# Kernel optimization log

Measured on AMD Instinct MI355X. Metric: run time of the kernel, lower is better.

The kernel has to match this reference:

```python
import jax, jax.numpy as jnp
import numpy as np

KH, KW = 3, 3
STRIDE = (1, 1)
PAD = (1, 1)
DIL = (1, 1)


def setup_inputs() -> dict:
    key = jax.random.key(0)
    k1, k2, k3, k4 = jax.random.split(key, 4)
    B, Cin, H, W = 8, 256, 64, 64
    Cout = 256
    x = jax.random.normal(k1, (B, Cin, H, W), jnp.float32)
    offset = jax.random.normal(k2, (B, 2 * KH * KW, H, W), jnp.float32)
    fan_in = Cin * KH * KW
    bound = 1.0 / np.sqrt(fan_in).astype(np.float32)
    weight = jax.random.uniform(k3, (Cout, Cin, KH, KW), jnp.float32, -bound, bound)
    bias = jax.random.uniform(k4, (Cout,), jnp.float32, -bound, bound)
    return {"x": x, "offset": offset, "weight": weight, "bias": bias}


def _deform_conv2d(x, offset, weight, bias):
    B, Cin, H, W = x.shape
    Cout = weight.shape[0]
    Ho, Wo = offset.shape[2], offset.shape[3]
    # offset layout: [B, 2*KH*KW, Ho, Wo] -> (dy, dx) per kernel tap
    off = offset.reshape(B, KH, KW, 2, Ho, Wo)
    dy = off[:, :, :, 0]  # [B,KH,KW,Ho,Wo]
    dx = off[:, :, :, 1]
    grid_y = jnp.arange(Ho, dtype=x.dtype) * STRIDE[0] - PAD[0]  # [Ho]
    grid_x = jnp.arange(Wo, dtype=x.dtype) * STRIDE[1] - PAD[1]  # [Wo]
    ker_y = jnp.arange(KH, dtype=x.dtype) * DIL[0]  # [KH]
    ker_x = jnp.arange(KW, dtype=x.dtype) * DIL[1]  # [KW]
    # sampling positions [B,KH,KW,Ho,Wo]
    py = dy + grid_y[None, None, None, :, None] + ker_y[None, :, None, None, None]
    px = dx + grid_x[None, None, None, None, :] + ker_x[None, None, :, None, None]

    y0f = jnp.floor(py)
    x0f = jnp.floor(px)
    wy = py - y0f  # fractional weights
    wx = px - x0f
    y0 = y0f.astype(jnp.int32)
    x0 = x0f.astype(jnp.int32)

    x_flat = x.reshape(B, Cin, H * W)

    def corner(yi, xi, w):
        # bilinear corner with zero padding outside the image
        valid = (yi >= 0) & (yi < H) & (xi >= 0) & (xi < W)
        idx = jnp.clip(yi, 0, H - 1) * W + jnp.clip(xi, 0, W - 1)  # [B,KH,KW,Ho,Wo]
        vals = jax.vmap(lambda xf, ii: xf[:, ii])(x_flat, idx)  # [B,Cin,KH,KW,Ho,Wo]
        return vals * (w * valid)[:, None]

    acc = corner(y0, x0, (1 - wy) * (1 - wx))
    acc = acc + corner(y0, x0 + 1, (1 - wy) * wx)
    acc = acc + corner(y0 + 1, x0, wy * (1 - wx))
    acc = acc + corner(y0 + 1, x0 + 1, wy * wx)

    # convolution accumulation over (Cin, KH, KW)
    out = jnp.einsum('bckluv,ockl->bouv', acc, weight)
    return out + bias[None, :, None, None]


def reference(x, offset, weight, bias):
    return _deform_conv2d(x, offset, weight, bias)
```

## Files before the change

### kernel.cpp

```cpp
#include <hip/hip_runtime.h>
#include <hip/hip_bf16.h>
#include <stdint.h>

typedef __attribute__((ext_vector_type(8))) short s16x8;
typedef __attribute__((ext_vector_type(4))) float f32x4;

#define XT_OFF   0u
#define WT_OFF   16777216u
#define PW_OFF   17956864u
#define PI_OFF   22675456u
#define WS_NEED  25034752u

static __device__ __forceinline__ uint16_t f2bf(float f) {
    __hip_bfloat16 h = __float2bfloat16(f);
    uint16_t u;
    __builtin_memcpy(&u, &h, 2);
    return u;
}
static __device__ __forceinline__ float bflo(uint32_t w) { return __uint_as_float(w << 16); }
static __device__ __forceinline__ float bfhi(uint32_t w) { return __uint_as_float(w & 0xffff0000u); }

__global__ __launch_bounds__(256) void k_transpose_x(const float* __restrict__ x,
                                                     uint16_t* __restrict__ xt) {
    __shared__ float tile[64][65];
    const int blk = blockIdx.x;
    const int b   = blk >> 8;
    const int yxt = (blk >> 2) & 63;
    const int ct  = blk & 3;
    const int yx0 = yxt << 6, c0 = ct << 6;
    const int tx  = threadIdx.x;
    const int ty  = tx >> 6, lx = tx & 63;
    #pragma unroll
    for (int i = 0; i < 16; ++i) {
        const int c = (i << 2) + ty;
        tile[c][lx] = x[(size_t)((b * 256 + c0 + c) << 12) + yx0 + lx];
    }
    __syncthreads();
    const int cpr = lx & 31;
    #pragma unroll
    for (int i = 0; i < 8; ++i) {
        const int r = (ty << 1) + (lx >> 5) + (i << 3);
        const uint32_t lo = f2bf(tile[2 * cpr][r]);
        const uint32_t hi = f2bf(tile[2 * cpr + 1][r]);
        *(uint32_t*)&xt[(size_t)(b * 4096 + yx0 + r) * 256 + c0 + 2 * cpr] = lo | (hi << 16);
    }
}

__global__ __launch_bounds__(256) void k_prep_w(const float* __restrict__ wgt,
                                                uint16_t* __restrict__ wt) {
    const int o = blockIdx.x;
    const int c = threadIdx.x;
    #pragma unroll
    for (int t = 0; t < 9; ++t) {
        const float v = wgt[(size_t)o * 2304 + c * 9 + t];
        const int kb = t * 8 + (c >> 5);
        const int kk = c & 31;
        const uint32_t byte = (uint32_t)kb * 16384u + (uint32_t)o * 64u
            + (uint32_t)(((((kk >> 3) ^ ((o >> 1) & 3)) << 4)) | ((kk & 7) << 1));
        wt[byte >> 1] = f2bf(v);
    }
}

__global__ __launch_bounds__(256) void k_prep_params(const float* __restrict__ off,
                                                     float4* __restrict__ pw,
                                                     uint2* __restrict__ pi) {
    const int blk = blockIdx.x;
    const int b = blk / 144;
    const int r = blk - b * 144;
    const int t = r >> 4;
    const int p = ((r & 15) << 8) + threadIdx.x;
    const int u = p >> 6, v = p & 63;
    const int kh = t / 3, kw = t - 3 * kh;
    const float dy = off[(size_t)((b * 18 + 2 * t) << 12) + p];
    const float dx = off[(size_t)((b * 18 + 2 * t + 1) << 12) + p];
    const float py = dy + (float)(u - 1 + kh);
    const float px = dx + (float)(v - 1 + kw);
    const float y0f = floorf(py), x0f = floorf(px);
    const float wy = py - y0f, wx = px - x0f;
    const int y0 = (int)y0f, x0 = (int)x0f;
    const int y1 = y0 + 1, x1 = x0 + 1;
    const bool vy0 = (y0 >= 0) && (y0 < 64);
    const bool vy1 = (y1 >= 0) && (y1 < 64);
    const bool vx0 = (x0 >= 0) && (x0 < 64);
    const bool vx1 = (x1 >= 0) && (x1 < 64);
    const int cy0 = min(max(y0, 0), 63), cy1 = min(max(y1, 0), 63);
    const int cx0 = min(max(x0, 0), 63), cx1 = min(max(x1, 0), 63);
    float4 w4;
    w4.x = (1.f - wy) * (1.f - wx) * ((vy0 && vx0) ? 1.f : 0.f);
    w4.y = (1.f - wy) * wx         * ((vy0 && vx1) ? 1.f : 0.f);
    w4.z = wy * (1.f - wx)         * ((vy1 && vx0) ? 1.f : 0.f);
    w4.w = wy * wx                 * ((vy1 && vx1) ? 1.f : 0.f);
    uint2 id;
    id.x = (uint32_t)(cy0 * 64 + cx0) | ((uint32_t)(cy0 * 64 + cx1) << 16);
    id.y = (uint32_t)(cy1 * 64 + cx0) | ((uint32_t)(cy1 * 64 + cx1) << 16);
    const size_t o_ = (size_t)(b * 9 + t) * 4096 + p;
    pw[o_] = w4;
    pi[o_] = id;
}

#define W_DMA(KB, BUF) do {                                                       \
    const char* gw_ = (const char*)wt + (size_t)(KB) * 16384u;                    \
    char* lw_ = (char*)&w_lds[BUF][0];                                            \
    _Pragma("unroll")                                                             \
    for (int it_ = 0; it_ < 2; ++it_) {                                           \
        const int seg_ = wv * 2 + it_;                                            \
        __builtin_amdgcn_global_load_lds(                                         \
            (const __attribute__((address_space(1))) void*)(gw_ + seg_ * 1024 + lane * 16), \
            (__attribute__((address_space(3))) void*)(lw_ + seg_ * 1024), 16, 0, 0); \
    }                                                                             \
} while (0)

__global__ __launch_bounds__(512, 4) void k_main(const uint16_t* __restrict__ xt,
                                                 const uint16_t* __restrict__ wt,
                                                 const float4* __restrict__ pw,
                                                 const uint2* __restrict__ pi,
                                                 const float* __restrict__ bias,
                                                 float* __restrict__ out) {
    __shared__ uint16_t w_lds[3][8192];
    __shared__ uint16_t im2col[64 * 256];

    const int orig = blockIdx.x;
    const int bid  = (orig & 7) * 64 + (orig >> 3);
    const int b    = bid >> 6;
    const int pix0 = (bid & 63) << 6;

    const int tx   = threadIdx.x;
    const int lane = tx & 63;
    const int wv   = tx >> 6;
    const int wc   = wv & 3;
    const int wp   = wv >> 2;
    const int l15  = lane & 15;
    const int kp   = lane >> 4;

    const int ar    = wc * 64 + l15;
    const int a_off = ar * 64 + ((kp ^ ((ar >> 1) & 3)) << 4);

    const uint16_t* xb = xt + (size_t)b * 4096 * 256;

    f32x4 acc[4][2];
    #pragma unroll
    for (int m = 0; m < 4; ++m)
        #pragma unroll
        for (int j = 0; j < 2; ++j) acc[m][j] = (f32x4){0.f, 0.f, 0.f, 0.f};

    W_DMA(0, 0);
    W_DMA(1, 1);

    for (int t = 0; t < 9; ++t) {
        __syncthreads();
        #pragma unroll
        for (int i = 0; i < 8; ++i) {
            const int lp = wv * 8 + i;
            const int uidx = __builtin_amdgcn_readfirstlane((b * 9 + t) * 4096 + pix0 + lp);
            const uint2  id = pi[uidx];
            const float4 w4 = pw[uidx];
            const uint16_t* p00 = xb + (id.x & 0xffffu) * 256u;
            const uint16_t* p01 = xb + (id.x >> 16)     * 256u;
            const uint16_t* p10 = xb + (id.y & 0xffffu) * 256u;
            const uint16_t* p11 = xb + (id.y >> 16)     * 256u;
            const uint2 A  = *(const uint2*)(p00 + lane * 4);
            const uint2 Bv = *(const uint2*)(p01 + lane * 4);
            const uint2 Cv = *(const uint2*)(p10 + lane * 4);
            const uint2 Dv = *(const uint2*)(p11 + lane * 4);
            uint2 r;
            {
                const float lo = w4.x * bflo(A.x) + w4.y * bflo(Bv.x)
                               + w4.z * bflo(Cv.x) + w4.w * bflo(Dv.x);
                const float hi = w4.x * bfhi(A.x) + w4.y * bfhi(Bv.x)
                               + w4.z * bfhi(Cv.x) + w4.w * bfhi(Dv.x);
                r.x = (uint32_t)f2bf(lo) | ((uint32_t)f2bf(hi) << 16);
            }
            {
                const float lo = w4.x * bflo(A.y) + w4.y * bflo(Bv.y)
                               + w4.z * bflo(Cv.y) + w4.w * bflo(Dv.y);
                const float hi = w4.x * bfhi(A.y) + w4.y * bfhi(Bv.y)
                               + w4.z * bfhi(Cv.y) + w4.w * bfhi(Dv.y);
                r.y = (uint32_t)f2bf(lo) | ((uint32_t)f2bf(hi) << 16);
            }
            const int slot = (lane >> 1) ^ (lp & 7);
            *(uint2*)((char*)im2col + lp * 512 + slot * 16 + (lane & 1) * 8) = r;
        }
        __syncthreads();

        #pragma unroll
        for (int s = 0; s < 8; ++s) {
            const int kb = t * 8 + s;
            if (t == 8 && s == 7) asm volatile("s_waitcnt vmcnt(0) lgkmcnt(0)" ::: "memory");
            else                  asm volatile("s_waitcnt vmcnt(2) lgkmcnt(0)" ::: "memory");
            __builtin_amdgcn_s_barrier();
            __builtin_amdgcn_sched_barrier(0);
            if (kb + 2 < 72) {
                const int ib = (kb + 2) % 3;
                W_DMA(kb + 2, ib);
            }
            const int cb = kb % 3;
            const char* wb = (const char*)&w_lds[cb][0];
            s16x8 afr[4], bfr[2];
            #pragma unroll
            for (int m = 0; m < 4; ++m) afr[m] = *(const s16x8*)(wb + a_off + m * 1024);
            #pragma unroll
            for (int j = 0; j < 2; ++j) {
                const int pix  = wp * 32 + j * 16 + l15;
                const int boff = pix * 512 + (((s * 4 + kp) ^ (l15 & 7)) << 4);
                bfr[j] = *(const s16x8*)((const char*)im2col + boff);
            }
            __builtin_amdgcn_s_setprio(1);
            #pragma unroll
            for (int m = 0; m < 4; ++m)
                #pragma unroll
                for (int j = 0; j < 2; ++j)
                    acc[m][j] = __builtin_amdgcn_mfma_f32_16x16x32_bf16(afr[m], bfr[j], acc[m][j], 0, 0, 0);
            __builtin_amdgcn_s_setprio(0);
        }
    }

    #pragma unroll
    for (int m = 0; m < 4; ++m) {
        #pragma unroll
        for (int q = 0; q < 4; ++q) {
            const int o = wc * 64 + m * 16 + kp * 4 + q;
            const float bv = bias[o];
            float* orow = out + (((size_t)(b * 256 + o)) << 12) + pix0 + wp * 32;
            #pragma unroll
            for (int j = 0; j < 2; ++j)
                orow[j * 16 + l15] = acc[m][j][q] + bv;
        }
    }
}

#define KTOT 2304
#define KCF  32
#define WROW 260
#define AROW 72

__global__ __launch_bounds__(256) void deform_conv_fallback(
    const float* __restrict__ x, const float* __restrict__ off,
    const float* __restrict__ wgt, const float* __restrict__ bias,
    float* __restrict__ out) {
    __shared__ float  w_lds[KCF][WROW];
    __shared__ float  a_lds[KCF][AROW];
    __shared__ int4   pidx[9][64];
    __shared__ float4 pwgt[9][64];
    const int tx = threadIdx.x;
    const int blk = blockIdx.x;
    const int b = blk >> 6, u = blk & 63;
    for (int item = tx; item < 9 * 64; item += 256) {
        const int t = item >> 6, p = item & 63;
        const int k = t / 3, l = t - 3 * k;
        const float dy = off[((b * 18 + 2 * t) << 12) + u * 64 + p];
        const float dx = off[((b * 18 + 2 * t + 1) << 12) + u * 64 + p];
        const float py = dy + (float)(u - 1 + k);
        const float px = dx + (float)(p - 1 + l);
        const float y0f = floorf(py), x0f = floorf(px);
        const float wy = py - y0f, wx = px - x0f;
        const int y0 = (int)y0f, x0 = (int)x0f, y1 = y0 + 1, x1 = x0 + 1;
        const bool vy0 = (y0 >= 0) && (y0 < 64), vy1 = (y1 >= 0) && (y1 < 64);
        const bool vx0 = (x0 >= 0) && (x0 < 64), vx1 = (x1 >= 0) && (x1 < 64);
        const int cy0 = min(max(y0, 0), 63), cy1 = min(max(y1, 0), 63);
        const int cx0 = min(max(x0, 0), 63), cx1 = min(max(x1, 0), 63);
        int4 id; id.x = cy0 * 64 + cx0; id.y = cy0 * 64 + cx1;
        id.z = cy1 * 64 + cx0; id.w = cy1 * 64 + cx1;
        float4 w4;
        w4.x = (1.f - wy) * (1.f - wx) * ((vy0 && vx0) ? 1.f : 0.f);
        w4.y = (1.f - wy) * wx * ((vy0 && vx1) ? 1.f : 0.f);
        w4.z = wy * (1.f - wx) * ((vy1 && vx0) ? 1.f : 0.f);
        w4.w = wy * wx * ((vy1 && vx1) ? 1.f : 0.f);
        pidx[t][p] = id; pwgt[t][p] = w4;
    }
    const int og = tx & 31, pgr = tx >> 5;
    float acc[8][8];
    #pragma unroll
    for (int j = 0; j < 8; ++j)
        #pragma unroll
        for (int q = 0; q < 8; ++q) acc[j][q] = 0.f;
    __syncthreads();
    for (int kb = 0; kb < 72; ++kb) {
        const int k0 = kb * KCF;
        #pragma unroll
        for (int it = 0; it < 8; ++it) {
            const int item = it * 256 + tx;
            const int o = item >> 3, jj = item & 7;
            const float4 v = *(const float4*)&wgt[o * KTOT + k0 + jj * 4];
            w_lds[jj * 4 + 0][o] = v.x; w_lds[jj * 4 + 1][o] = v.y;
            w_lds[jj * 4 + 2][o] = v.z; w_lds[jj * 4 + 3][o] = v.w;
        }
        #pragma unroll
        for (int it = 0; it < 8; ++it) {
            const int item = it * 256 + tx;
            const int kk = item >> 6, p = item & 63;
            const int kg = k0 + kk;
            const int c = kg / 9, t = kg - 9 * c;
            const float* plane = x + ((b * 256 + c) << 12);
            const int4 id = pidx[t][p];
            const float4 w4 = pwgt[t][p];
            float v = w4.x * plane[id.x] + w4.y * plane[id.y]
                    + w4.z * plane[id.z] + w4.w * plane[id.w];
            a_lds[kk][p] = v;
        }
        __syncthreads();
        #pragma unroll 2
        for (int kk = 0; kk < KCF; ++kk) {
            const float4 w0 = *(const float4*)&w_lds[kk][og * 8];
            const float4 w1 = *(const float4*)&w_lds[kk][og * 8 + 4];
            const float4 a0 = *(const float4*)&a_lds[kk][pgr * 8];
            const float4 a1 = *(const float4*)&a_lds[kk][pgr * 8 + 4];
            const float wv[8] = {w0.x, w0.y, w0.z, w0.w, w1.x, w1.y, w1.z, w1.w};
            const float av[8] = {a0.x, a0.y, a0.z, a0.w, a1.x, a1.y, a1.z, a1.w};
            #pragma unroll
            for (int j = 0; j < 8; ++j)
                #pragma unroll
                for (int q = 0; q < 8; ++q) acc[j][q] += wv[j] * av[q];
        }
        __syncthreads();
    }
    const int vb = pgr * 8;
    #pragma unroll
    for (int j = 0; j < 8; ++j) {
        const int o = og * 8 + j;
        const float bv = bias[o];
        float* op = out + ((b * 256 + o) << 12) + u * 64 + vb;
        float4 r0, r1;
        r0.x = acc[j][0] + bv; r0.y = acc[j][1] + bv; r0.z = acc[j][2] + bv; r0.w = acc[j][3] + bv;
        r1.x = acc[j][4] + bv; r1.y = acc[j][5] + bv; r1.z = acc[j][6] + bv; r1.w = acc[j][7] + bv;
        *(float4*)op = r0; *(float4*)(op + 4) = r1;
    }
}

extern "C" void kernel_launch(void* const* d_in, const int* in_sizes, int n_in,
                              void* d_out, int out_size, void* d_ws, size_t ws_size,
                              hipStream_t stream) {
    const float* x    = (const float*)d_in[0];
    const float* off  = (const float*)d_in[1];
    const float* wgt  = (const float*)d_in[2];
    const float* bias = (const float*)d_in[3];
    float* out = (float*)d_out;

    if (ws_size < WS_NEED) {
        deform_conv_fallback<<<dim3(512), dim3(256), 0, stream>>>(x, off, wgt, bias, out);
        return;
    }
    uint16_t* xt  = (uint16_t*)((char*)d_ws + XT_OFF);
    uint16_t* wtp = (uint16_t*)((char*)d_ws + WT_OFF);
    float4*   pwp = (float4*)((char*)d_ws + PW_OFF);
    uint2*    pip = (uint2*)((char*)d_ws + PI_OFF);

    k_transpose_x <<<dim3(2048), dim3(256), 0, stream>>>(x, xt);
    k_prep_w      <<<dim3(256),  dim3(256), 0, stream>>>(wgt, wtp);
    k_prep_params <<<dim3(1152), dim3(256), 0, stream>>>(off, pwp, pip);
    k_main        <<<dim3(512),  dim3(512), 0, stream>>>(xt, wtp, pwp, pip, bias, out);
}
```

Baseline: 98.86 us.

## Software-pipeline bilinear gather for next tap behind current tap's MFMA steps

Reorganizes the main loop so the parameter loads and four-corner gathers for tap t+1 are issued in bursts interleaved with the eight MFMA k-steps of tap t. Blended results are held in registers and written to the single im2col buffer after a barrier at the end of each tap. The aim is to hide gather latency and remove the exposed two-barrier gather phase per tap. In exchange it adds many live registers under a 512x4 launch bound, which risks spills, and it relies on hand-tuned vmcnt values that must match the exact load counts.

```diff
diff --git a/kernel.cpp b/kernel.cpp
--- a/kernel.cpp
+++ b/kernel.cpp
@@ -110,6 +110,82 @@
     }                                                                             \
 } while (0)
 
+#define KSTEP(KB, N) do {                                                         \
+    asm volatile("s_waitcnt vmcnt(" #N ") lgkmcnt(0)" ::: "memory");              \
+    __builtin_amdgcn_s_barrier();                                                 \
+    __builtin_amdgcn_sched_barrier(0);                                            \
+    if ((KB) + 2 < 72) W_DMA((KB) + 2, ((KB) + 2) % 3);                           \
+    {                                                                             \
+        const int s_ = (KB) & 7;                                                  \
+        const char* wb_ = (const char*)&w_lds[(KB) % 3][0];                       \
+        s16x8 afr[4], bfr[2];                                                     \
+        _Pragma("unroll")                                                         \
+        for (int m = 0; m < 4; ++m) afr[m] = *(const s16x8*)(wb_ + a_off + m * 1024); \
+        _Pragma("unroll")                                                         \
+        for (int j = 0; j < 2; ++j) {                                             \
+            const int pix_  = wp * 32 + j * 16 + l15;                             \
+            const int boff_ = pix_ * 512 + (((s_ * 4 + kp) ^ (l15 & 7)) << 4);    \
+            bfr[j] = *(const s16x8*)((const char*)im2col + boff_);                \
+        }                                                                         \
+        __builtin_amdgcn_s_setprio(1);                                            \
+        _Pragma("unroll")                                                         \
+        for (int m = 0; m < 4; ++m)                                               \
+            _Pragma("unroll")                                                     \
+            for (int j = 0; j < 2; ++j)                                           \
+                acc[m][j] = __builtin_amdgcn_mfma_f32_16x16x32_bf16(afr[m], bfr[j], acc[m][j], 0, 0, 0); \
+        __builtin_amdgcn_s_setprio(0);                                            \
+    }                                                                             \
+} while (0)
+
+#define CBURST(P0) do {                                                           \
+    _Pragma("unroll")                                                             \
+    for (int i = 0; i < 4; ++i) {                                                 \
+        const uint2 id_ = pin[(P0) + i];                                          \
+        cA[i] = *(const uint2*)(xb + (id_.x & 0xffffu) * 256u + lane * 4);        \
+        cB[i] = *(const uint2*)(xb + (id_.x >> 16)     * 256u + lane * 4);        \
+        cC[i] = *(const uint2*)(xb + (id_.y & 0xffffu) * 256u + lane * 4);        \
+        cD[i] = *(const uint2*)(xb + (id_.y >> 16)     * 256u + lane * 4);        \
+    }                                                                             \
+} while (0)
+
+#define CBLEND(P0) do {                                                           \
+    _Pragma("unroll")                                                             \
+    for (int i = 0; i < 4; ++i) {                                                 \
+        const float4 w4_ = pwn[(P0) + i];                                         \
+        uint2 r_;                                                                 \
+        { const float lo = w4_.x * bflo(cA[i].x) + w4_.y * bflo(cB[i].x)          \
+                         + w4_.z * bflo(cC[i].x) + w4_.w * bflo(cD[i].x);         \
+          const float hi = w4_.x * bfhi(cA[i].x) + w4_.y * bfhi(cB[i].x)          \
+                         + w4_.z * bfhi(cC[i].x) + w4_.w * bfhi(cD[i].x);         \
+          r_.x = (uint32_t)f2bf(lo) | ((uint32_t)f2bf(hi) << 16); }               \
+        { const float lo = w4_.x * bflo(cA[i].y) + w4_.y * bflo(cB[i].y)          \
+                         + w4_.z * bflo(cC[i].y) + w4_.w * bflo(cD[i].y);         \
+          const float hi = w4_.x * bfhi(cA[i].y) + w4_.y * bfhi(cB[i].y)          \
+                         + w4_.z * bfhi(cC[i].y) + w4_.w * bfhi(cD[i].y);         \
+          r_.y = (uint32_t)f2bf(lo) | ((uint32_t)f2bf(hi) << 16); }               \
+        rr[(P0) + i] = r_;                                                        \
+    }                                                                             \
+} while (0)
+
+#define LOAD_PARAMS(TT) do {                                                      \
+    _Pragma("unroll")                                                             \
+    for (int i = 0; i < 8; ++i) {                                                 \
+        const int lp_ = wv * 8 + i;                                               \
+        const int ui_ = __builtin_amdgcn_readfirstlane((b * 9 + (TT)) * 4096 + pix0 + lp_); \
+        pin[i] = pi[ui_];                                                         \
+        pwn[i] = pw[ui_];                                                         \
+    }                                                                             \
+} while (0)
+
+#define DS_WRITE_RR() do {                                                        \
+    _Pragma("unroll")                                                             \
+    for (int i = 0; i < 8; ++i) {                                                 \
+        const int lp_ = wv * 8 + i;                                               \
+        const int slot_ = (lane >> 1) ^ (lp_ & 7);                                \
+        *(uint2*)((char*)im2col + lp_ * 512 + slot_ * 16 + (lane & 1) * 8) = rr[i]; \
+    }                                                                             \
+} while (0)
+
 __global__ __launch_bounds__(512, 4) void k_main(const uint16_t* __restrict__ xt,
                                                  const uint16_t* __restrict__ wt,
                                                  const float4* __restrict__ pw,
@@ -137,82 +213,53 @@
 
     const uint16_t* xb = xt + (size_t)b * 4096 * 256;
 
+    uint2  pin[8];
+    float4 pwn[8];
+    uint2  cA[4], cB[4], cC[4], cD[4];
+    uint2  rr[8];
+
     f32x4 acc[4][2];
     #pragma unroll
     for (int m = 0; m < 4; ++m)
         #pragma unroll
         for (int j = 0; j < 2; ++j) acc[m][j] = (f32x4){0.f, 0.f, 0.f, 0.f};
 
+    LOAD_PARAMS(0);
+    CBURST(0);
+    asm volatile("s_waitcnt vmcnt(0)" ::: "memory");
+    CBLEND(0);
+    CBURST(4);
     W_DMA(0, 0);
     W_DMA(1, 1);
-
-    for (int t = 0; t < 9; ++t) {
-        __syncthreads();
-        #pragma unroll
-        for (int i = 0; i < 8; ++i) {
-            const int lp = wv * 8 + i;
-            const int uidx = __builtin_amdgcn_readfirstlane((b * 9 + t) * 4096 + pix0 + lp);
-            const uint2  id = pi[uidx];
-            const float4 w4 = pw[uidx];
-            const uint16_t* p00 = xb + (id.x & 0xffffu) * 256u;
-            const uint16_t* p01 = xb + (id.x >> 16)     * 256u;
-            const uint16_t* p10 = xb + (id.y & 0xffffu) * 256u;
-            const uint16_t* p11 = xb + (id.y >> 16)     * 256u;
-            const uint2 A  = *(const uint2*)(p00 + lane * 4);
-            const uint2 Bv = *(const uint2*)(p01 + lane * 4);
-            const uint2 Cv = *(const uint2*)(p10 + lane * 4);
-            const uint2 Dv = *(const uint2*)(p11 + lane * 4);
-            uint2 r;
-            {
-                const float lo = w4.x * bflo(A.x) + w4.y * bflo(Bv.x)
-                               + w4.z * bflo(Cv.x) + w4.w * bflo(Dv.x);
-                const float hi = w4.x * bfhi(A.x) + w4.y * bfhi(Bv.x)
-                               + w4.z * bfhi(Cv.x) + w4.w * bfhi(Dv.x);
-                r.x = (uint32_t)f2bf(lo) | ((uint32_t)f2bf(hi) << 16);
-            }
-            {
-                const float lo = w4.x * bflo(A.y) + w4.y * bflo(Bv.y)
-                               + w4.z * bflo(Cv.y) + w4.w * bflo(Dv.y);
-                const float hi = w4.x * bfhi(A.y) + w4.y * bfhi(Bv.y)
-                               + w4.z * bfhi(Cv.y) + w4.w * bfhi(Dv.y);
-                r.y = (uint32_t)f2bf(lo) | ((uint32_t)f2bf(hi) << 16);
-            }
-            const int slot = (lane >> 1) ^ (lp & 7);
-            *(uint2*)((char*)im2col + lp * 512 + slot * 16 + (lane & 1) * 8) = r;
-        }
-        __syncthreads();
-
-        #pragma unroll
-        for (int s = 0; s < 8; ++s) {
-            const int kb = t * 8 + s;
-            if (t == 8 && s == 7) asm volatile("s_waitcnt vmcnt(0) lgkmcnt(0)" ::: "memory");
-            else                  asm volatile("s_waitcnt vmcnt(2) lgkmcnt(0)" ::: "memory");
-            __builtin_amdgcn_s_barrier();
-            __builtin_amdgcn_sched_barrier(0);
-            if (kb + 2 < 72) {
-                const int ib = (kb + 2) % 3;
-                W_DMA(kb + 2, ib);
-            }
-            const int cb = kb % 3;
-            const char* wb = (const char*)&w_lds[cb][0];
-            s16x8 afr[4], bfr[2];
-            #pragma unroll
-            for (int m = 0; m < 4; ++m) afr[m] = *(const s16x8*)(wb + a_off + m * 1024);
-            #pragma unroll
-            for (int j = 0; j < 2; ++j) {
-                const int pix  = wp * 32 + j * 16 + l15;
-                const int boff = pix * 512 + (((s * 4 + kp) ^ (l15 & 7)) << 4);
-                bfr[j] = *(const s16x8*)((const char*)im2col + boff);
-            }
-            __builtin_amdgcn_s_setprio(1);
-            #pragma unroll
-            for (int m = 0; m < 4; ++m)
-                #pragma unroll
-                for (int j = 0; j < 2; ++j)
-                    acc[m][j] = __builtin_amdgcn_mfma_f32_16x16x32_bf16(afr[m], bfr[j], acc[m][j], 0, 0, 0);
-            __builtin_amdgcn_s_setprio(0);
-        }
-    }
+    asm volatile("s_waitcnt vmcnt(4)" ::: "memory");
+    CBLEND(4);
+    DS_WRITE_RR();
+
+    #pragma unroll 1
+    for (int t = 0; t < 8; ++t) {
+        LOAD_PARAMS(t + 1);
+        CBURST(0);
+        KSTEP(t * 8 + 0, 18);
+        KSTEP(t * 8 + 1, 18);
+        KSTEP(t * 8 + 2, 2);
+        KSTEP(t * 8 + 3, 2);
+        asm volatile("s_waitcnt vmcnt(4)" ::: "memory");
+        CBLEND(0);
+        CBURST(4);
+        KSTEP(t * 8 + 4, 18);
+        KSTEP(t * 8 + 5, 18);
+        KSTEP(t * 8 + 6, 2);
+        KSTEP(t * 8 + 7, 2);
+        asm volatile("s_waitcnt vmcnt(4)" ::: "memory");
+        CBLEND(4);
+        asm volatile("s_waitcnt lgkmcnt(0)" ::: "memory");
+        __builtin_amdgcn_s_barrier();
+        __builtin_amdgcn_sched_barrier(0);
+        DS_WRITE_RR();
+    }
+
+    KSTEP(64, 2); KSTEP(65, 2); KSTEP(66, 2); KSTEP(67, 2);
+    KSTEP(68, 2); KSTEP(69, 2); KSTEP(70, 2); KSTEP(71, 0);
 
     #pragma unroll
     for (int m = 0; m < 4; ++m) {
```

Measured after the change: 115.8 us. +17.2%, slower.

## Software-pipeline deformable gather with MFMA, load weights directly into registers

Applied to the files above, without the earlier changes.

The main kernel is restructured so each block covers 128 pixels with a double-buffered im2col in LDS. The bilinear gather and blend for the next kernel tap is interleaved with the MFMA steps of the current tap, which removes the serial gather-then-compute phases. Weights are pre-packed into MFMA fragment order, so each wave loads its A fragments straight from global memory into registers instead of staging them through LDS with DMA. This larger tile raises per-thread register use and halves the grid to 256 blocks, trading occupancy for more reuse and overlap.

```diff
diff --git a/kernel.cpp b/kernel.cpp
--- a/kernel.cpp
+++ b/kernel.cpp
@@ -19,6 +19,9 @@
 }
 static __device__ __forceinline__ float bflo(uint32_t w) { return __uint_as_float(w << 16); }
 static __device__ __forceinline__ float bfhi(uint32_t w) { return __uint_as_float(w & 0xffff0000u); }
+static __device__ __forceinline__ float rdl(float v, int l) {
+    return __uint_as_float((uint32_t)__builtin_amdgcn_readlane((int)__float_as_uint(v), l));
+}
 
 __global__ __launch_bounds__(256) void k_transpose_x(const float* __restrict__ x,
                                                      uint16_t* __restrict__ xt) {
@@ -48,17 +51,21 @@
 
 __global__ __launch_bounds__(256) void k_prep_w(const float* __restrict__ wgt,
                                                 uint16_t* __restrict__ wt) {
-    const int o = blockIdx.x;
-    const int c = threadIdx.x;
-    #pragma unroll
-    for (int t = 0; t < 9; ++t) {
-        const float v = wgt[(size_t)o * 2304 + c * 9 + t];
-        const int kb = t * 8 + (c >> 5);
-        const int kk = c & 31;
-        const uint32_t byte = (uint32_t)kb * 16384u + (uint32_t)o * 64u
-            + (uint32_t)(((((kk >> 3) ^ ((o >> 1) & 3)) << 4)) | ((kk & 7) << 1));
-        wt[byte >> 1] = f2bf(v);
-    }
+    const int blk = blockIdx.x;
+    const int kb = blk >> 2, wc = blk & 3;
+    const int m = threadIdx.x >> 6, lane = threadIdx.x & 63;
+    const int o = wc * 64 + m * 16 + (lane & 15);
+    const int t = kb >> 3;
+    const int ch0 = (kb & 7) * 32 + (lane >> 4) * 8;
+    uint32_t pk[4];
+    #pragma unroll
+    for (int q = 0; q < 4; ++q) {
+        const float v0 = wgt[(size_t)o * 2304 + (size_t)(ch0 + 2 * q) * 9 + t];
+        const float v1 = wgt[(size_t)o * 2304 + (size_t)(ch0 + 2 * q + 1) * 9 + t];
+        pk[q] = (uint32_t)f2bf(v0) | ((uint32_t)f2bf(v1) << 16);
+    }
+    uint4 r; r.x = pk[0]; r.y = pk[1]; r.z = pk[2]; r.w = pk[3];
+    *(uint4*)((char*)wt + (size_t)kb * 16384 + wc * 4096 + m * 1024 + lane * 16) = r;
 }
 
 __global__ __launch_bounds__(256) void k_prep_params(const float* __restrict__ off,
@@ -98,120 +105,158 @@
     pi[o_] = id;
 }
 
-#define W_DMA(KB, BUF) do {                                                       \
-    const char* gw_ = (const char*)wt + (size_t)(KB) * 16384u;                    \
-    char* lw_ = (char*)&w_lds[BUF][0];                                            \
-    _Pragma("unroll")                                                             \
-    for (int it_ = 0; it_ < 2; ++it_) {                                           \
-        const int seg_ = wv * 2 + it_;                                            \
-        __builtin_amdgcn_global_load_lds(                                         \
-            (const __attribute__((address_space(1))) void*)(gw_ + seg_ * 1024 + lane * 16), \
-            (__attribute__((address_space(3))) void*)(lw_ + seg_ * 1024), 16, 0, 0); \
+
+#define BLENDPX(PAR, IDX, LP, PXL) do {                                           \
+    const float wqa = rdl(pwv.x, (PXL)), wqb = rdl(pwv.y, (PXL));                 \
+    const float wqc = rdl(pwv.z, (PXL)), wqd = rdl(pwv.w, (PXL));                 \
+    const uint2 A_ = cr[PAR][(IDX)*4+0], B_ = cr[PAR][(IDX)*4+1];                 \
+    const uint2 C_ = cr[PAR][(IDX)*4+2], D_ = cr[PAR][(IDX)*4+3];                 \
+    uint2 r_;                                                                     \
+    { const float lo = wqa * bflo(A_.x) + wqb * bflo(B_.x)                        \
+                     + wqc * bflo(C_.x) + wqd * bflo(D_.x);                       \
+      const float hi = wqa * bfhi(A_.x) + wqb * bfhi(B_.x)                        \
+                     + wqc * bfhi(C_.x) + wqd * bfhi(D_.x);                       \
+      r_.x = (uint32_t)f2bf(lo) | ((uint32_t)f2bf(hi) << 16); }                   \
+    { const float lo = wqa * bflo(A_.y) + wqb * bflo(B_.y)                        \
+                     + wqc * bflo(C_.y) + wqd * bflo(D_.y);                       \
+      const float hi = wqa * bfhi(A_.y) + wqb * bfhi(B_.y)                        \
+                     + wqc * bfhi(C_.y) + wqd * bfhi(D_.y);                       \
+      r_.y = (uint32_t)f2bf(lo) | ((uint32_t)f2bf(hi) << 16); }                   \
+    const int slot_ = (lane >> 1) ^ ((LP) & 7);                                   \
+    *(uint2*)(inxt + (LP) * 512 + slot_ * 16 + (lane & 1) * 8) = r_;              \
+} while (0)
+
+#define STEP(T, S, STG) do {                                                      \
+    const int kb_ = (T) * 8 + (S);                                                \
+    if (STG) {                                                                    \
+        const uint32_t ixA = (uint32_t)__builtin_amdgcn_readlane((int)piv.x, 2*(S));     \
+        const uint32_t iyA = (uint32_t)__builtin_amdgcn_readlane((int)piv.y, 2*(S));     \
+        const uint32_t ixB = (uint32_t)__builtin_amdgcn_readlane((int)piv.x, 2*(S)+1);   \
+        const uint32_t iyB = (uint32_t)__builtin_amdgcn_readlane((int)piv.y, 2*(S)+1);   \
+        cr[(S)&1][0] = *(const uint2*)(xb + (ixA & 0xffffu) * 256u + lane * 4);   \
+        cr[(S)&1][1] = *(const uint2*)(xb + (ixA >> 16)     * 256u + lane * 4);   \
+        cr[(S)&1][2] = *(const uint2*)(xb + (iyA & 0xffffu) * 256u + lane * 4);   \
+        cr[(S)&1][3] = *(const uint2*)(xb + (iyA >> 16)     * 256u + lane * 4);   \
+        cr[(S)&1][4] = *(const uint2*)(xb + (ixB & 0xffffu) * 256u + lane * 4);   \
+        cr[(S)&1][5] = *(const uint2*)(xb + (ixB >> 16)     * 256u + lane * 4);   \
+        cr[(S)&1][6] = *(const uint2*)(xb + (iyB & 0xffffu) * 256u + lane * 4);   \
+        cr[(S)&1][7] = *(const uint2*)(xb + (iyB >> 16)     * 256u + lane * 4);   \
+    }                                                                             \
+    if (kb_ < 71) {                                                               \
+        _Pragma("unroll")                                                         \
+        for (int m = 0; m < 4; ++m)                                               \
+            wA[((S)+1)&1][m] = *(const s16x8*)(wfrag + (size_t)(kb_+1) * 16384 + m * 1024); \
+    }                                                                             \
+    if ((STG) && (S) >= 1) {                                                      \
+        BLENDPX(((S)-1)&1, 0, wv * 16 + 2*((S)-1),     2*((S)-1));                \
+        BLENDPX(((S)-1)&1, 1, wv * 16 + 2*((S)-1) + 1, 2*((S)-1)+1);              \
+    }                                                                             \
+    {                                                                             \
+        s16x8 bfr[4];                                                             \
+        _Pragma("unroll")                                                         \
+        for (int j = 0; j < 4; ++j)                                               \
+            bfr[j] = *(const s16x8*)(icur + rb0 + j * 8192 + so[S]);              \
+        __builtin_amdgcn_s_setprio(1);                                            \
+        _Pragma("unroll")                                                         \
+        for (int m = 0; m < 4; ++m)                                               \
+            _Pragma("unroll")                                                     \
+            for (int j = 0; j < 4; ++j)                                           \
+                acc[m][j] = __builtin_amdgcn_mfma_f32_16x16x32_bf16(wA[(S)&1][m], bfr[j], acc[m][j], 0, 0, 0); \
+        __builtin_amdgcn_s_setprio(0);                                            \
     }                                                                             \
 } while (0)
 
-__global__ __launch_bounds__(512, 4) void k_main(const uint16_t* __restrict__ xt,
+__global__ __launch_bounds__(512, 2) void k_main(const uint16_t* __restrict__ xt,
                                                  const uint16_t* __restrict__ wt,
                                                  const float4* __restrict__ pw,
                                                  const uint2* __restrict__ pi,
                                                  const float* __restrict__ bias,
                                                  float* __restrict__ out) {
-    __shared__ uint16_t w_lds[3][8192];
-    __shared__ uint16_t im2col[64 * 256];
+    __shared__ uint16_t imc[2][128 * 256];
 
     const int orig = blockIdx.x;
-    const int bid  = (orig & 7) * 64 + (orig >> 3);
-    const int b    = bid >> 6;
-    const int pix0 = (bid & 63) << 6;
+    const int bid  = (orig & 7) * 32 + (orig >> 3);
+    const int b    = bid >> 5;
+    const int pix0 = (bid & 31) << 7;
 
     const int tx   = threadIdx.x;
     const int lane = tx & 63;
     const int wv   = tx >> 6;
     const int wc   = wv & 3;
-    const int wp   = wv >> 2;
+    const int wn   = wv >> 2;
     const int l15  = lane & 15;
     const int kp   = lane >> 4;
 
-    const int ar    = wc * 64 + l15;
-    const int a_off = ar * 64 + ((kp ^ ((ar >> 1) & 3)) << 4);
-
     const uint16_t* xb = xt + (size_t)b * 4096 * 256;
-
-    f32x4 acc[4][2];
+    const char* wfrag = (const char*)wt + (size_t)wc * 4096 + (size_t)lane * 16;
+
+    int so[8];
+    #pragma unroll
+    for (int s = 0; s < 8; ++s) so[s] = ((s * 4 + kp) ^ (l15 & 7)) << 4;
+    const int rb0 = (wn * 64 + l15) * 512;
+
+    f32x4 acc[4][4];
     #pragma unroll
     for (int m = 0; m < 4; ++m)
         #pragma unroll
-        for (int j = 0; j < 2; ++j) acc[m][j] = (f32x4){0.f, 0.f, 0.f, 0.f};
-
-    W_DMA(0, 0);
-    W_DMA(1, 1);
-
-    for (int t = 0; t < 9; ++t) {
+        for (int j = 0; j < 4; ++j) acc[m][j] = (f32x4){0.f, 0.f, 0.f, 0.f};
+
+    #pragma unroll
+    for (int i = 0; i < 16; ++i) {
+        const int lp = wv * 16 + i;
+        const int ui = __builtin_amdgcn_readfirstlane(b * 9 * 4096 + pix0 + lp);
+        const uint2  id = pi[ui];
+        const float4 w4 = pw[ui];
+        const uint2 A  = *(const uint2*)(xb + (id.x & 0xffffu) * 256u + lane * 4);
+        const uint2 Bv = *(const uint2*)(xb + (id.x >> 16)     * 256u + lane * 4);
+        const uint2 Cv = *(const uint2*)(xb + (id.y & 0xffffu) * 256u + lane * 4);
+        const uint2 Dv = *(const uint2*)(xb + (id.y >> 16)     * 256u + lane * 4);
+        uint2 r;
+        { const float lo = w4.x * bflo(A.x) + w4.y * bflo(Bv.x)
+                         + w4.z * bflo(Cv.x) + w4.w * bflo(Dv.x);
+          const float hi = w4.x * bfhi(A.x) + w4.y * bfhi(Bv.x)
+                         + w4.z * bfhi(Cv.x) + w4.w * bfhi(Dv.x);
+          r.x = (uint32_t)f2bf(lo) | ((uint32_t)f2bf(hi) << 16); }
+        { const float lo = w4.x * bflo(A.y) + w4.y * bflo(Bv.y)
+                         + w4.z * bflo(Cv.y) + w4.w * bflo(Dv.y);
+          const float hi = w4.x * bfhi(A.y) + w4.y * bfhi(Bv.y)
+                         + w4.z * bfhi(Cv.y) + w4.w * bfhi(Dv.y);
+          r.y = (uint32_t)f2bf(lo) | ((uint32_t)f2bf(hi) << 16); }
+        const int slot = (lane >> 1) ^ (lp & 7);
+        *(uint2*)((char*)&imc[0][0] + lp * 512 + slot * 16 + (lane & 1) * 8) = r;
+    }
+
+    s16x8 wA[2][4];
+    #pragma unroll
+    for (int m = 0; m < 4; ++m) wA[0][m] = *(const s16x8*)(wfrag + m * 1024);
+
+    uint2  cr[2][8];
+    uint2  piv = {0, 0};
+    float4 pwv = {0.f, 0.f, 0.f, 0.f};
+
+    #pragma unroll 1
+    for (int t = 0; t < 8; ++t) {
         __syncthreads();
-        #pragma unroll
-        for (int i = 0; i < 8; ++i) {
-            const int lp = wv * 8 + i;
-            const int uidx = __builtin_amdgcn_readfirstlane((b * 9 + t) * 4096 + pix0 + lp);
-            const uint2  id = pi[uidx];
-            const float4 w4 = pw[uidx];
-            const uint16_t* p00 = xb + (id.x & 0xffffu) * 256u;
-            const uint16_t* p01 = xb + (id.x >> 16)     * 256u;
-            const uint16_t* p10 = xb + (id.y & 0xffffu) * 256u;
-            const uint16_t* p11 = xb + (id.y >> 16)     * 256u;
-            const uint2 A  = *(const uint2*)(p00 + lane * 4);
-            const uint2 Bv = *(const uint2*)(p01 + lane * 4);
-            const uint2 Cv = *(const uint2*)(p10 + lane * 4);
-            const uint2 Dv = *(const uint2*)(p11 + lane * 4);
-            uint2 r;
-            {
-                const float lo = w4.x * bflo(A.x) + w4.y * bflo(Bv.x)
-                               + w4.z * bflo(Cv.x) + w4.w * bflo(Dv.x);
-                const float hi = w4.x * bfhi(A.x) + w4.y * bfhi(Bv.x)
-                               + w4.z * bfhi(Cv.x) + w4.w * bfhi(Dv.x);
-                r.x = (uint32_t)f2bf(lo) | ((uint32_t)f2bf(hi) << 16);
-            }
-            {
-                const float lo = w4.x * bflo(A.y) + w4.y * bflo(Bv.y)
-                               + w4.z * bflo(Cv.y) + w4.w * bflo(Dv.y);
-                const float hi = w4.x * bfhi(A.y) + w4.y * bfhi(Bv.y)
-                               + w4.z * bfhi(Cv.y) + w4.w * bfhi(Dv.y);
-                r.y = (uint32_t)f2bf(lo) | ((uint32_t)f2bf(hi) << 16);
-            }
-            const int slot = (lane >> 1) ^ (lp & 7);
-            *(uint2*)((char*)im2col + lp * 512 + slot * 16 + (lane & 1) * 8) = r;
-        }
-        __syncthreads();
-
-        #pragma unroll
-        for (int s = 0; s < 8; ++s) {
-            const int kb = t * 8 + s;
-            if (t == 8 && s == 7) asm volatile("s_waitcnt vmcnt(0) lgkmcnt(0)" ::: "memory");
-            else                  asm volatile("s_waitcnt vmcnt(2) lgkmcnt(0)" ::: "memory");
-            __builtin_amdgcn_s_barrier();
-            __builtin_amdgcn_sched_barrier(0);
-            if (kb + 2 < 72) {
-                const int ib = (kb + 2) % 3;
-                W_DMA(kb + 2, ib);
-            }
-            const int cb = kb % 3;
-            const char* wb = (const char*)&w_lds[cb][0];
-            s16x8 afr[4], bfr[2];
-            #pragma unroll
-            for (int m = 0; m < 4; ++m) afr[m] = *(const s16x8*)(wb + a_off + m * 1024);
-            #pragma unroll
-            for (int j = 0; j < 2; ++j) {
-                const int pix  = wp * 32 + j * 16 + l15;
-                const int boff = pix * 512 + (((s * 4 + kp) ^ (l15 & 7)) << 4);
-                bfr[j] = *(const s16x8*)((const char*)im2col + boff);
-            }
-            __builtin_amdgcn_s_setprio(1);
-            #pragma unroll
-            for (int m = 0; m < 4; ++m)
-                #pragma unroll
-                for (int j = 0; j < 2; ++j)
-                    acc[m][j] = __builtin_amdgcn_mfma_f32_16x16x32_bf16(afr[m], bfr[j], acc[m][j], 0, 0, 0);
-            __builtin_amdgcn_s_setprio(0);
-        }
+        const char* icur = (const char*)&imc[t & 1][0];
+        char*       inxt = (char*)&imc[(t + 1) & 1][0];
+        {
+            const int idx = (b * 9 + t + 1) * 4096 + pix0 + wv * 16 + l15;
+            piv = pi[idx];
+            pwv = pw[idx];
+        }
+        STEP(t, 0, 1); STEP(t, 1, 1); STEP(t, 2, 1); STEP(t, 3, 1);
+        STEP(t, 4, 1); STEP(t, 5, 1); STEP(t, 6, 1); STEP(t, 7, 1);
+        BLENDPX(1, 0, wv * 16 + 14, 14);
+        BLENDPX(1, 1, wv * 16 + 15, 15);
+    }
+
+    __syncthreads();
+    {
+        const char* icur = (const char*)&imc[0][0];
+        char*       inxt = (char*)&imc[1][0];
+        (void)inxt;
+        STEP(8, 0, 0); STEP(8, 1, 0); STEP(8, 2, 0); STEP(8, 3, 0);
+        STEP(8, 4, 0); STEP(8, 5, 0); STEP(8, 6, 0); STEP(8, 7, 0);
     }
 
     #pragma unroll
@@ -220,9 +265,9 @@
         for (int q = 0; q < 4; ++q) {
             const int o = wc * 64 + m * 16 + kp * 4 + q;
             const float bv = bias[o];
-            float* orow = out + (((size_t)(b * 256 + o)) << 12) + pix0 + wp * 32;
+            float* orow = out + (((size_t)(b * 256 + o)) << 12) + pix0 + wn * 64;
             #pragma unroll
-            for (int j = 0; j < 2; ++j)
+            for (int j = 0; j < 4; ++j)
                 orow[j * 16 + l15] = acc[m][j][q] + bv;
         }
     }
@@ -345,7 +390,7 @@
     uint2*    pip = (uint2*)((char*)d_ws + PI_OFF);
 
     k_transpose_x <<<dim3(2048), dim3(256), 0, stream>>>(x, xt);
-    k_prep_w      <<<dim3(256),  dim3(256), 0, stream>>>(wgt, wtp);
+    k_prep_w      <<<dim3(288),  dim3(256), 0, stream>>>(wgt, wtp);
     k_prep_params <<<dim3(1152), dim3(256), 0, stream>>>(off, pwp, pip);
-    k_main        <<<dim3(512),  dim3(512), 0, stream>>>(xt, wtp, pwp, pip, bias, out);
-}
+    k_main        <<<dim3(256),  dim3(512), 0, stream>>>(xt, wtp, pwp, pip, bias, out);
+}
```

Result: faster. 85.38 us (-13.6%).
